# Performance work log

Measured on AMD Instinct MI355X. Metric: run time of the kernel, lower is better.

## Reference

```python
import jax, jax.numpy as jnp
import numpy as np

N0, N1, N2 = 60000, 15000, 3750
K, P = 32, 15
R0 = 0.5  # kernel extent at level 0; doubles per level (first_subsampling_dl*deform_radius scaled to unit-cube data)


def kpconv(q_pts, s_pts, neigh_idx, feats, kpoints, W, extent):
    """Rigid KPConv. q_pts [Nq,3], s_pts [Ns,3], neigh_idx [Nq,K] (shadow=Ns),
    feats [Ns,Cin], kpoints [P,3] unit-scale, W [P,Cin,Cout]."""
    s_pts_p = jnp.concatenate([s_pts, jnp.full((1, 3), 1e6, s_pts.dtype)], 0)
    feats_p = jnp.concatenate([feats, jnp.zeros((1, feats.shape[1]), feats.dtype)], 0)
    neigh_pts = s_pts_p[neigh_idx]                       # [Nq,K,3] gather
    neigh_f = feats_p[neigh_idx]                         # [Nq,K,Cin] gather
    diff = neigh_pts - q_pts[:, None, :]                 # [Nq,K,3]
    dist = jnp.sqrt(jnp.sum((diff[:, :, None, :] - kpoints[None, None] * extent) ** 2, -1))
    infl = jnp.maximum(0.0, 1.0 - dist / extent)         # [Nq,K,P] linear influence
    fk = jnp.einsum('nkp,nkc->npc', infl, neigh_f)       # per-kernel-point aggregation
    out = jnp.einsum('npc,pco->no', fk, W)
    return jax.nn.leaky_relu(out, 0.1)


def detection_scores(neighbor, features):
    # verbatim translation of KPFCNN.detection_scores (eval mode)
    n_total = features.shape[0]
    feats = jnp.concatenate([features, jnp.zeros_like(features[:1])], 0)
    neighbor = jnp.concatenate([neighbor, jnp.full_like(neighbor[:1], n_total)], 0)
    feats = feats / (jnp.max(feats) + 1e-6)
    nf = feats[neighbor]                                 # [N+1,K,C]
    nnum = jnp.maximum(jnp.sum(jnp.sum(nf, -1) != 0, -1, keepdims=True), 1)
    mean_f = jnp.sum(nf, 1) / nnum
    local_max_score = jax.nn.softplus(feats - mean_f)
    depth_max = jnp.max(feats, 1, keepdims=True)
    all_scores = local_max_score * (feats / (1e-6 + depth_max))
    scores = jnp.max(all_scores, 1, keepdims=True)
    detected = jnp.max((feats == jnp.max(nf, 1)).astype(feats.dtype), 1, keepdims=True)
    return (scores * detected)[:-1]


def reference(features, points0, points1, points2, neighbors0, neighbors1, neighbors2,
              pools0, pools1, upsamples0, upsamples1, kpoints, W1, W2, W3, W4, W5, Wu1, Wu2):
    # ---- encoder ----
    f = kpconv(points0, points0, neighbors0, features, kpoints, W1, R0)      # simple         [N0,64]
    skip0 = f
    f = kpconv(points1, points0, pools0, f, kpoints, W2, R0)                 # simple_strided [N1,64]
    f = kpconv(points1, points1, neighbors1, f, kpoints, W3, 2 * R0)         # simple         [N1,128]
    skip1 = f
    f = kpconv(points2, points1, pools1, f, kpoints, W4, 2 * R0)             # simple_strided [N2,128]
    f = kpconv(points2, points2, neighbors2, f, kpoints, W5, 4 * R0)         # simple         [N2,256]
    # ---- decoder: nearest_upsample + skip concat + unary ----
    f = jnp.concatenate([f[upsamples1[:, 0]], skip1], 1)                     # [N1,384] (1.5*256)
    f = jax.nn.leaky_relu(f @ Wu1, 0.1)                                      # unary          [N1,128]
    f = jnp.concatenate([f[upsamples0[:, 0]], skip0], 1)                     # [N0,192]
    f = f @ Wu2                                                              # last_unary     [N0,32]
    scores = detection_scores(neighbors0, f)
    fnorm = f / jnp.maximum(jnp.linalg.norm(f, axis=-1, keepdims=True), 1e-12)
    return fnorm, scores


def setup_inputs() -> dict:
    key = jax.random.key(0)
    ks = jax.random.split(key, 20)
    inp = {
        'features': jax.random.normal(ks[0], (N0, 1), jnp.float32),
        'points0': jax.random.uniform(ks[1], (N0, 3), jnp.float32),
        'points1': jax.random.uniform(ks[2], (N1, 3), jnp.float32),
        'points2': jax.random.uniform(ks[3], (N2, 3), jnp.float32),
        'neighbors0': jax.random.randint(ks[4], (N0, K), 0, N0, jnp.int32),
        'neighbors1': jax.random.randint(ks[5], (N1, K), 0, N1, jnp.int32),
        'neighbors2': jax.random.randint(ks[6], (N2, K), 0, N2, jnp.int32),
        'pools0': jax.random.randint(ks[7], (N1, K), 0, N0, jnp.int32),
        'pools1': jax.random.randint(ks[8], (N2, K), 0, N1, jnp.int32),
        'upsamples0': jax.random.randint(ks[9], (N0, 1), 0, N1, jnp.int32),
        'upsamples1': jax.random.randint(ks[10], (N1, 1), 0, N2, jnp.int32),
        'kpoints': jax.random.normal(ks[11], (P, 3), jnp.float32) * 0.5,
    }
    def w(k, shape, fan_in):
        return jax.random.normal(k, shape, jnp.float32) / np.sqrt(fan_in)
    inp['W1'] = w(ks[12], (P, 1, 64), P * 1)
    inp['W2'] = w(ks[13], (P, 64, 64), P * 64)
    inp['W3'] = w(ks[14], (P, 64, 128), P * 64)
    inp['W4'] = w(ks[15], (P, 128, 128), P * 128)
    inp['W5'] = w(ks[16], (P, 128, 256), P * 128)
    inp['Wu1'] = w(ks[17], (384, 128), 384)
    inp['Wu2'] = w(ks[18], (192, 32), 192)
    return inp
```

## Files before the change

### kernel.cpp

```cpp
#include <hip/hip_runtime.h>
#include <math.h>

static const int cN0 = 60000;
static const int cN1 = 15000;
static const int cN2 = 3750;

typedef __bf16 bf16x8 __attribute__((ext_vector_type(8)));
typedef float f32x4 __attribute__((ext_vector_type(4)));

#define GLOAD_LDS16(gsrc, ldst)                                                        \
  __builtin_amdgcn_global_load_lds((const __attribute__((address_space(1))) void*)(gsrc), \
                                   (__attribute__((address_space(3))) void*)(ldst), 16, 0, 0)

__global__ __launch_bounds__(256) void prep_kernel(
    const float* __restrict__ pts0, const float* __restrict__ feat,
    const float* __restrict__ pts1, const float* __restrict__ pts2,
    const float* __restrict__ W2, const float* __restrict__ W3, const float* __restrict__ W4,
    const float* __restrict__ W5, const float* __restrict__ Wu1, const float* __restrict__ Wu2,
    float4* __restrict__ pk0, float4* __restrict__ pk1, float4* __restrict__ pk2,
    __bf16* __restrict__ T2, __bf16* __restrict__ T3, __bf16* __restrict__ T4,
    __bf16* __restrict__ T5, __bf16* __restrict__ Tu1, __bf16* __restrict__ Tu2) {
  int role = blockIdx.y;
  int tid = blockIdx.x * 256 + threadIdx.x;
  int stride = gridDim.x * 256;
  if (role < 3) {
    const float* p = role == 0 ? pts0 : (role == 1 ? pts1 : pts2);
    float4* o = role == 0 ? pk0 : (role == 1 ? pk1 : pk2);
    int n = role == 0 ? cN0 : (role == 1 ? cN1 : cN2);
    for (int i = tid; i < n; i += stride) {
      float4 v;
      v.x = p[(size_t)i * 3 + 0];
      v.y = p[(size_t)i * 3 + 1];
      v.z = p[(size_t)i * 3 + 2];
      v.w = role == 0 ? feat[i] : 0.f;
      o[i] = v;
    }
  } else {
    const float* src;
    __bf16* dst;
    int Kd, Nd;
    switch (role) {
      case 3: src = W2;  dst = T2;  Kd = 960;  Nd = 64;  break;
      case 4: src = W3;  dst = T3;  Kd = 960;  Nd = 128; break;
      case 5: src = W4;  dst = T4;  Kd = 1920; Nd = 128; break;
      case 6: src = W5;  dst = T5;  Kd = 1920; Nd = 256; break;
      case 7: src = Wu1; dst = Tu1; Kd = 384;  Nd = 128; break;
      default: src = Wu2; dst = Tu2; Kd = 192; Nd = 32;  break;
    }
    int total = Kd * Nd;
    for (int e = tid; e < total; e += stride) {
      int n = e / Kd, k = e % Kd;
      dst[e] = (__bf16)src[(size_t)k * Nd + n];
    }
  }
}

__global__ __launch_bounds__(256) void kpconv_l1(
    const float4* __restrict__ pk, const int* __restrict__ neigh,
    const float* __restrict__ kpts, const float* __restrict__ W1,
    __bf16* __restrict__ f0, float extent) {
  const int t = threadIdx.x;
  const int n0b = blockIdx.x * 16;
  __shared__ float s_nb[32][16][4];
  __shared__ float s_fk[16][16];
  __shared__ float s_W[960];
  for (int i = t; i < 960; i += 256) s_W[i] = W1[i];
  #pragma unroll
  for (int i = 0; i < 2; ++i) {
    int e = t + i * 256;
    int pt = e & 15, k = e >> 4;
    int idx = neigh[(size_t)(n0b + pt) * 32 + k];
    *(float4*)&s_nb[k][pt][0] = pk[idx];
  }
  __syncthreads();
  const int lane = t & 63, wave = t >> 6;
  const int g = lane >> 4, p_raw = lane & 15;
  const int p = p_raw < 15 ? p_raw : 0;
  const int pt = wave * 4 + g;
  const int n = n0b + pt;
  const float inv = 1.f / extent;
  float4 q = pk[n];
  const float kx = q.x + kpts[p * 3 + 0] * extent;
  const float ky = q.y + kpts[p * 3 + 1] * extent;
  const float kz = q.z + kpts[p * 3 + 2] * extent;
  float fk = 0.f;
  #pragma unroll 8
  for (int k = 0; k < 32; ++k) {
    f32x4 rec = *(const f32x4*)&s_nb[k][pt][0];
    float dx = rec[0] - kx, dy = rec[1] - ky, dz = rec[2] - kz;
    float d = sqrtf(dx * dx + dy * dy + dz * dz);
    fk += fmaxf(0.f, 1.f - d * inv) * rec[3];
  }
  if (p_raw < 15) s_fk[pt][p_raw] = fk;
  __syncthreads();
  #pragma unroll
  for (int o = 0; o < 4; ++o) {
    int e = o * 256 + t;
    int opt = e >> 6, c = e & 63;
    float acc = 0.f;
    #pragma unroll
    for (int pp = 0; pp < 15; ++pp) acc += s_fk[opt][pp] * s_W[pp * 64 + c];
    acc = acc > 0.f ? acc : 0.1f * acc;
    f0[(size_t)(n0b + opt) * 64 + c] = (__bf16)acc;
  }
}

template <int CIN, int PTS>
__global__ __launch_bounds__(256) void kpconv_agg_mfma(
    const float4* __restrict__ qp, const float4* __restrict__ sp,
    const int* __restrict__ neigh, const __bf16* __restrict__ F,
    const float* __restrict__ kpts, __bf16* __restrict__ fkb,
    int M, float extent) {
  constexpr int ROWS = PTS * 32;
  constexpr int TPR = 256 / ROWS;
  constexpr int CPT = CIN / (8 * TPR);
  constexpr int NCC = CIN / 16;
  constexpr int PPW = PTS / 4;
  __shared__ __bf16 s_F[PTS][32][CIN];
  __shared__ __bf16 s_infl[PTS][16][40];
  const int t = threadIdx.x;
  const int rowid = t / TPR, half = t % TPR;
  const int pt = rowid >> 5, k = rowid & 31;
  const int n = blockIdx.x * PTS + pt;
  const int n_eff = n < M ? n : M - 1;
  const int idx = neigh[(size_t)n_eff * 32 + k];
  {
    const __bf16* src = F + (size_t)idx * CIN + half * (CIN / TPR);
    __bf16* dst = &s_F[pt][k][half * (CIN / TPR)];
    #pragma unroll
    for (int j = 0; j < CPT; ++j) *(bf16x8*)(dst + j * 8) = *(const bf16x8*)(src + j * 8);
  }
  {
    float4 q = qp[n_eff];
    float4 s = sp[idx];
    float sx = s.x - q.x, sy = s.y - q.y, sz = s.z - q.z;
    float inv = 1.f / extent;
    #pragma unroll
    for (int p = 0; p < 15; ++p) {
      float dx = sx - kpts[p * 3 + 0] * extent;
      float dy = sy - kpts[p * 3 + 1] * extent;
      float dz = sz - kpts[p * 3 + 2] * extent;
      float d = sqrtf(dx * dx + dy * dy + dz * dz);
      s_infl[pt][p][k] = (__bf16)fmaxf(0.f, 1.f - d * inv);
    }
  }
  __syncthreads();
  const int lane = t & 63, wave = t >> 6;
  const int g = lane >> 4, c16 = lane & 15;
  #pragma unroll
  for (int qq = 0; qq < PPW; ++qq) {
    const int lpt = wave * PPW + qq;
    const int nn = blockIdx.x * PTS + lpt;
    bf16x8 a = *(const bf16x8*)&s_infl[lpt][c16][g * 8];
    if (nn < M) {
      const size_t base = (size_t)nn * (15 * CIN);
      #pragma unroll
      for (int cc = 0; cc < NCC; ++cc) {
        bf16x8 b;
        #pragma unroll
        for (int j = 0; j < 8; ++j) b[j] = s_F[lpt][g * 8 + j][cc * 16 + c16];
        f32x4 acc = __builtin_amdgcn_mfma_f32_16x16x32_bf16(a, b, (f32x4){0.f, 0.f, 0.f, 0.f}, 0, 0, 0);
        #pragma unroll
        for (int r = 0; r < 4; ++r) {
          int p = g * 4 + r;
          if (p < 15) fkb[base + (size_t)p * CIN + cc * 16 + c16] = (__bf16)acc[r];
        }
      }
    }
  }
}

template <bool LEAKY, bool GATHER, bool OUTF32, bool MAXOUT>
__global__ __launch_bounds__(256, 2) void gemm_mfma(
    const __bf16* __restrict__ A1, const __bf16* __restrict__ A2,
    const int* __restrict__ gidx, const int K1,
    const __bf16* __restrict__ BT, void* __restrict__ Cout,
    const int M, const int N, const int KK, unsigned* __restrict__ gmax) {
  __shared__ __bf16 sA[2][4096];
  __shared__ __bf16 sB[2][4096];
  __shared__ float s_max[4];
  const int t = threadIdx.x;
  const int lane = t & 63, wave = t >> 6;
  const int wr = wave >> 1, wc = wave & 1;
  const int m0 = blockIdx.y * 64, n0 = blockIdx.x * 64;
  const int K2 = KK - K1;

  const __bf16* a1row[2];
  const __bf16* a2row[2];
  const __bf16* brow_[2];
  int csrc[2], wbase[2];
  #pragma unroll
  for (int r = 0; r < 2; ++r) {
    int slot = r * 256 + wave * 64 + lane;
    int row = slot >> 3;
    csrc[r] = ((slot & 7) ^ (row & 7)) * 8;
    wbase[r] = (r * 256 + wave * 64) * 8;
    int gm = m0 + row; if (gm > M - 1) gm = M - 1;
    if (GATHER) {
      a1row[r] = A1 + (size_t)gidx[gm] * K1;
      a2row[r] = A2 + (size_t)gm * (size_t)K2;
    } else {
      a1row[r] = A1 + (size_t)gm * (size_t)KK;
    }
    int gn = n0 + row; if (gn > N - 1) gn = N - 1;
    brow_[r] = BT + (size_t)gn * (size_t)KK;
  }

  int offA[2][2], offB[2][2];
  #pragma unroll
  for (int i = 0; i < 2; ++i)
    #pragma unroll
    for (int s = 0; s < 2; ++s) {
      int ra = wr * 32 + i * 16 + (lane & 15);
      int rb = wc * 32 + i * 16 + (lane & 15);
      int ch = s * 4 + (lane >> 4);
      offA[i][s] = ra * 64 + (ch ^ (ra & 7)) * 8;
      offB[i][s] = rb * 64 + (ch ^ (rb & 7)) * 8;
    }

  f32x4 acc[2][2];
  #pragma unroll
  for (int i = 0; i < 2; ++i)
    #pragma unroll
    for (int j = 0; j < 2; ++j) acc[i][j] = (f32x4){0.f, 0.f, 0.f, 0.f};

  auto stage = [&](int buf, int k0) {
    #pragma unroll
    for (int r = 0; r < 2; ++r) {
      int kg = k0 + csrc[r];
      const __bf16* asrc;
      if (GATHER) asrc = (kg < K1) ? (a1row[r] + kg) : (a2row[r] + (kg - K1));
      else        asrc = a1row[r] + kg;
      GLOAD_LDS16(asrc, &sA[buf][wbase[r]]);
      GLOAD_LDS16(brow_[r] + kg, &sB[buf][wbase[r]]);
    }
  };

  stage(0, 0);
  __syncthreads();
  const int nk = KK >> 6;
  int cur = 0;
  for (int kt = 0; kt < nk; ++kt) {
    if (kt + 1 < nk) stage(cur ^ 1, (kt + 1) << 6);
    #pragma unroll
    for (int s = 0; s < 2; ++s) {
      bf16x8 a0 = *(const bf16x8*)&sA[cur][offA[0][s]];
      bf16x8 a1 = *(const bf16x8*)&sA[cur][offA[1][s]];
      bf16x8 b0 = *(const bf16x8*)&sB[cur][offB[0][s]];
      bf16x8 b1 = *(const bf16x8*)&sB[cur][offB[1][s]];
      acc[0][0] = __builtin_amdgcn_mfma_f32_16x16x32_bf16(a0, b0, acc[0][0], 0, 0, 0);
      acc[0][1] = __builtin_amdgcn_mfma_f32_16x16x32_bf16(a0, b1, acc[0][1], 0, 0, 0);
      acc[1][0] = __builtin_amdgcn_mfma_f32_16x16x32_bf16(a1, b0, acc[1][0], 0, 0, 0);
      acc[1][1] = __builtin_amdgcn_mfma_f32_16x16x32_bf16(a1, b1, acc[1][1], 0, 0, 0);
    }
    __syncthreads();
    cur ^= 1;
  }

  float lmax = 0.f;
  #pragma unroll
  for (int i = 0; i < 2; ++i)
    #pragma unroll
    for (int j = 0; j < 2; ++j)
      #pragma unroll
      for (int g = 0; g < 4; ++g) {
        int row = m0 + wr * 32 + i * 16 + (lane >> 4) * 4 + g;
        int col = n0 + wc * 32 + j * 16 + (lane & 15);
        if (row < M && col < N) {
          float v = acc[i][j][g];
          if (LEAKY) v = v > 0.f ? v : 0.1f * v;
          if (MAXOUT) lmax = fmaxf(lmax, v);
          if (OUTF32) ((float*)Cout)[(size_t)row * N + col] = v;
          else        ((__bf16*)Cout)[(size_t)row * N + col] = (__bf16)v;
        }
      }
  if (MAXOUT) {
    #pragma unroll
    for (int s = 32; s >= 1; s >>= 1) lmax = fmaxf(lmax, __shfl_xor(lmax, s, 64));
    if (lane == 0) s_max[wave] = lmax;
    __syncthreads();
    if (t == 0) {
      float mm = fmaxf(fmaxf(s_max[0], s_max[1]), fmaxf(s_max[2], s_max[3]));
      atomicMax(gmax, __float_as_uint(mm));
    }
  }
}

__global__ __launch_bounds__(256) void detect_kernel(
    const float* __restrict__ f6, const int* __restrict__ neigh,
    const float* __restrict__ gm_ptr, float* __restrict__ out_fnorm,
    float* __restrict__ out_scores, int N) {
  int n = blockIdx.x * 8 + (threadIdx.x >> 5);
  int c = threadIdx.x & 31;
  if (n >= N) return;
  float denom = gm_ptr[0] + 1e-6f;
  float fown = f6[(size_t)n * 32 + c];
  int idx_l = neigh[(size_t)n * 32 + c];
  float colsum = 0.f, colmax = -1e30f;
  for (int k = 0; k < 32; ++k) {
    int idx = __shfl(idx_l, k, 32);
    float v = f6[(size_t)idx * 32 + c];
    colsum += v;
    colmax = fmaxf(colmax, v);
  }
  float fs = fown / denom;
  float mean = (colsum / denom) * (1.f / 32.f);
  float x = fs - mean;
  float lms = fmaxf(x, 0.f) + log1pf(expf(-fabsf(x)));
  float dm = fs;
  #pragma unroll
  for (int s = 16; s >= 1; s >>= 1) dm = fmaxf(dm, __shfl_xor(dm, s, 32));
  float as = lms * fs / (1e-6f + dm);
  float sc = as;
  #pragma unroll
  for (int s = 16; s >= 1; s >>= 1) sc = fmaxf(sc, __shfl_xor(sc, s, 32));
  float det = (fown == colmax) ? 1.f : 0.f;
  #pragma unroll
  for (int s = 16; s >= 1; s >>= 1) det = fmaxf(det, __shfl_xor(det, s, 32));
  float nn2 = fown * fown;
  #pragma unroll
  for (int s = 16; s >= 1; s >>= 1) nn2 += __shfl_xor(nn2, s, 32);
  float inv_nrm = 1.f / fmaxf(sqrtf(nn2), 1e-12f);
  out_fnorm[(size_t)n * 32 + c] = fown * inv_nrm;
  if (c == 0) out_scores[n] = sc * det;
}

extern "C" void kernel_launch(void* const* d_in, const int* in_sizes, int n_in,
                              void* d_out, int out_size, void* d_ws, size_t ws_size,
                              hipStream_t stream) {
  const float* features  = (const float*)d_in[0];
  const float* points0   = (const float*)d_in[1];
  const float* points1   = (const float*)d_in[2];
  const float* points2   = (const float*)d_in[3];
  const int* neighbors0  = (const int*)d_in[4];
  const int* neighbors1  = (const int*)d_in[5];
  const int* neighbors2  = (const int*)d_in[6];
  const int* pools0      = (const int*)d_in[7];
  const int* pools1      = (const int*)d_in[8];
  const int* upsamples0  = (const int*)d_in[9];
  const int* upsamples1  = (const int*)d_in[10];
  const float* kpoints   = (const float*)d_in[11];
  const float* W1  = (const float*)d_in[12];
  const float* W2  = (const float*)d_in[13];
  const float* W3  = (const float*)d_in[14];
  const float* W4  = (const float*)d_in[15];
  const float* W5  = (const float*)d_in[16];
  const float* Wu1 = (const float*)d_in[17];
  const float* Wu2 = (const float*)d_in[18];

  const float R0 = 0.5f;

  char* wp = (char*)d_ws;
  auto alloc = [&](size_t bytes) {
    char* r = wp;
    wp += (bytes + 255) & ~(size_t)255;
    return r;
  };
  __bf16* f0b  = (__bf16*)alloc((size_t)cN0 * 64 * 2);
  __bf16* f1b  = (__bf16*)alloc((size_t)cN1 * 64 * 2);
  __bf16* f2b  = (__bf16*)alloc((size_t)cN1 * 128 * 2);
  __bf16* f3b  = (__bf16*)alloc((size_t)cN2 * 128 * 2);
  __bf16* f4b  = (__bf16*)alloc((size_t)cN2 * 256 * 2);
  __bf16* f5b  = (__bf16*)alloc((size_t)cN1 * 128 * 2);
  float*  f6   = (float*)alloc((size_t)cN0 * 32 * 4);
  __bf16* WT2  = (__bf16*)alloc(960 * 64 * 2);
  __bf16* WT3  = (__bf16*)alloc(960 * 128 * 2);
  __bf16* WT4  = (__bf16*)alloc(1920 * 128 * 2);
  __bf16* WT5  = (__bf16*)alloc(1920 * 256 * 2);
  __bf16* WTu1 = (__bf16*)alloc(384 * 128 * 2);
  __bf16* WTu2 = (__bf16*)alloc(192 * 32 * 2);
  unsigned* gm = (unsigned*)alloc(256);
  float4* pk0  = (float4*)alloc((size_t)cN0 * 16);
  float4* pk1  = (float4*)alloc((size_t)cN1 * 16);
  float4* pk2  = (float4*)alloc((size_t)cN2 * 16);
  __bf16* fkb  = (__bf16*)alloc((size_t)cN1 * 960 * 2);

  prep_kernel<<<dim3(240, 9), 256, 0, stream>>>(
      points0, features, points1, points2, W2, W3, W4, W5, Wu1, Wu2,
      pk0, pk1, pk2, WT2, WT3, WT4, WT5, WTu1, WTu2);
  kpconv_l1<<<cN0 / 16, 256, 0, stream>>>(pk0, neighbors0, kpoints, W1, f0b, R0);

  kpconv_agg_mfma<64, 8><<<cN1 / 8, 256, 0, stream>>>(pk1, pk0, pools0, f0b, kpoints, fkb, cN1, R0);
  gemm_mfma<true, false, false, false><<<dim3(1, 235), 256, 0, stream>>>(
      fkb, nullptr, nullptr, 0, WT2, f1b, cN1, 64, 960, nullptr);
  kpconv_agg_mfma<64, 8><<<cN1 / 8, 256, 0, stream>>>(pk1, pk1, neighbors1, f1b, kpoints, fkb, cN1, 2.f * R0);
  gemm_mfma<true, false, false, false><<<dim3(2, 235), 256, 0, stream>>>(
      fkb, nullptr, nullptr, 0, WT3, f2b, cN1, 128, 960, nullptr);
  kpconv_agg_mfma<128, 4><<<(cN2 + 3) / 4, 256, 0, stream>>>(pk2, pk1, pools1, f2b, kpoints, fkb, cN2, 2.f * R0);
  gemm_mfma<true, false, false, false><<<dim3(2, 59), 256, 0, stream>>>(
      fkb, nullptr, nullptr, 0, WT4, f3b, cN2, 128, 1920, nullptr);
  kpconv_agg_mfma<128, 4><<<(cN2 + 3) / 4, 256, 0, stream>>>(pk2, pk2, neighbors2, f3b, kpoints, fkb, cN2, 4.f * R0);
  gemm_mfma<true, false, false, false><<<dim3(4, 59), 256, 0, stream>>>(
      fkb, nullptr, nullptr, 0, WT5, f4b, cN2, 256, 1920, nullptr);
  gemm_mfma<true, true, false, false><<<dim3(2, 235), 256, 0, stream>>>(
      f4b, f2b, upsamples1, 256, WTu1, f5b, cN1, 128, 384, nullptr);
  hipMemsetAsync(gm, 0, 4, stream);
  gemm_mfma<false, true, true, true><<<dim3(1, 938), 256, 0, stream>>>(
      f5b, f0b, upsamples0, 128, WTu2, f6, cN0, 32, 192, gm);

  float* out_fnorm = (float*)d_out;
  float* out_scores = out_fnorm + (size_t)cN0 * 32;
  detect_kernel<<<(cN0 + 7) / 8, 256, 0, stream>>>(f6, neighbors0, (const float*)gm,
                                                   out_fnorm, out_scores, cN0);
}
```

Before: 224.6 us.

## Fuse KPConv aggregation and weight GEMM into one kernel per layer

```diff
diff --git a/kernel.cpp b/kernel.cpp
--- a/kernel.cpp
+++ b/kernel.cpp
@@ -105,69 +105,214 @@
   }
 }
 
-template <int CIN, int PTS>
-__global__ __launch_bounds__(256) void kpconv_agg_mfma(
+template <int CIN, int COUT, int BM, bool BDBUF>
+__global__ __launch_bounds__(512) void kpconv_fused(
     const float4* __restrict__ qp, const float4* __restrict__ sp,
     const int* __restrict__ neigh, const __bf16* __restrict__ F,
-    const float* __restrict__ kpts, __bf16* __restrict__ fkb,
-    int M, float extent) {
-  constexpr int ROWS = PTS * 32;
-  constexpr int TPR = 256 / ROWS;
-  constexpr int CPT = CIN / (8 * TPR);
-  constexpr int NCC = CIN / 16;
-  constexpr int PPW = PTS / 4;
-  __shared__ __bf16 s_F[PTS][32][CIN];
-  __shared__ __bf16 s_infl[PTS][16][40];
+    const float* __restrict__ kpts, const __bf16* __restrict__ BT,
+    __bf16* __restrict__ out, int M, float extent) {
+  constexpr int KK = 15 * CIN;
+  constexpr int KT = KK / 64;
+  constexpr int CPRow = CIN / 8;
+  constexpr int RPB = 8192 / CIN;
+  constexpr int GS = RPB / 2;
+  constexpr int BP = RPB / 32;
+  constexpr int NB = BM * 32 / RPB;
+  constexpr int WPP = 8 / BP;
+  constexpr int FBUF = 8192;
+  constexpr int RG = BM / 16;
+  constexpr int CG = 8 / RG;
+  constexpr int NJ = COUT / (16 * CG);
+  constexpr int SMEM_FK = BM * KK * 2;
+  constexpr int SMEM = SMEM_FK + BP * 1280 + BM * 16 + 2 * FBUF * 2;
+
+  __shared__ __align__(16) char smem[SMEM];
+  __bf16* s_fk   = (__bf16*)smem;
+  __bf16* s_infl = (__bf16*)(smem + SMEM_FK);
+  float4* s_q    = (float4*)(smem + SMEM_FK + BP * 1280);
+  __bf16* s_F    = (__bf16*)(smem + SMEM_FK + BP * 1280 + BM * 16);
+  __bf16* s_B    = s_F;
+
   const int t = threadIdx.x;
-  const int rowid = t / TPR, half = t % TPR;
-  const int pt = rowid >> 5, k = rowid & 31;
-  const int n = blockIdx.x * PTS + pt;
-  const int n_eff = n < M ? n : M - 1;
-  const int idx = neigh[(size_t)n_eff * 32 + k];
-  {
-    const __bf16* src = F + (size_t)idx * CIN + half * (CIN / TPR);
-    __bf16* dst = &s_F[pt][k][half * (CIN / TPR)];
-    #pragma unroll
-    for (int j = 0; j < CPT; ++j) *(bf16x8*)(dst + j * 8) = *(const bf16x8*)(src + j * 8);
-  }
-  {
-    float4 q = qp[n_eff];
-    float4 s = sp[idx];
-    float sx = s.x - q.x, sy = s.y - q.y, sz = s.z - q.z;
-    float inv = 1.f / extent;
-    #pragma unroll
-    for (int p = 0; p < 15; ++p) {
-      float dx = sx - kpts[p * 3 + 0] * extent;
-      float dy = sy - kpts[p * 3 + 1] * extent;
-      float dz = sz - kpts[p * 3 + 2] * extent;
+  const int w = t >> 6, l = t & 63;
+  const int c16 = l & 15, g4 = l >> 4;
+  const int m0 = blockIdx.x * BM;
+  const int* nb_base = neigh + (size_t)m0 * 32;
+  int rlim = (M - m0) * 32 - 1;
+  if (rlim > BM * 32 - 1) rlim = BM * 32 - 1;
+
+  const int gb = t / CPRow;
+  const int ch = t % CPRow;
+  int idxg[NB][2];
+  #pragma unroll
+  for (int b = 0; b < NB; ++b)
+    #pragma unroll
+    for (int j = 0; j < 2; ++j) {
+      int r = b * RPB + gb + j * GS;
+      idxg[b][j] = nb_base[r < rlim ? r : rlim];
+    }
+  const int ii  = t & 1;
+  const int pq4 = ((t >> 1) & 3) * 4;
+  const int row_i = gb + ii * GS;
+  const int pt_i = row_i >> 5, kk_i = row_i & 31;
+  const float inv = 1.f / extent;
+  float kpx[4], kpy[4], kpz[4];
+  #pragma unroll
+  for (int pi = 0; pi < 4; ++pi) {
+    int p = pq4 + pi; if (p > 14) p = 14;
+    kpx[pi] = kpts[p * 3 + 0] * extent;
+    kpy[pi] = kpts[p * 3 + 1] * extent;
+    kpz[pi] = kpts[p * 3 + 2] * extent;
+  }
+  if (t < BM) { int n = m0 + t; s_q[t] = qp[n < M ? n : M - 1]; }
+
+  auto stageF = [&](int buf, const int (&ig)[2]) {
+    #pragma unroll
+    for (int j = 0; j < 2; ++j) {
+      int k = (gb + j * GS) & 31;
+      const __bf16* src = F + (size_t)ig[j] * CIN + (ch ^ ((k >> 3) & 3)) * 8;
+      GLOAD_LDS16(src, s_F + buf * FBUF + (j * 512 + t) * 8);
+    }
+  };
+  auto inflC = [&](const float4& spv, int b, float (&v)[4]) {
+    float4 q = s_q[b * BP + pt_i];
+    float sx = spv.x - q.x, sy = spv.y - q.y, sz = spv.z - q.z;
+    #pragma unroll
+    for (int pi = 0; pi < 4; ++pi) {
+      float dx = sx - kpx[pi], dy = sy - kpy[pi], dz = sz - kpz[pi];
       float d = sqrtf(dx * dx + dy * dy + dz * dz);
-      s_infl[pt][p][k] = (__bf16)fmaxf(0.f, 1.f - d * inv);
-    }
-  }
-  __syncthreads();
-  const int lane = t & 63, wave = t >> 6;
-  const int g = lane >> 4, c16 = lane & 15;
-  #pragma unroll
-  for (int qq = 0; qq < PPW; ++qq) {
-    const int lpt = wave * PPW + qq;
-    const int nn = blockIdx.x * PTS + lpt;
-    bf16x8 a = *(const bf16x8*)&s_infl[lpt][c16][g * 8];
-    if (nn < M) {
-      const size_t base = (size_t)nn * (15 * CIN);
+      v[pi] = fmaxf(0.f, 1.f - d * inv);
+    }
+  };
+  auto inflStore = [&](const float (&v)[4]) {
+    #pragma unroll
+    for (int pi = 0; pi < 4; ++pi) {
+      int p = pq4 + pi;
+      if (p < 15) s_infl[pt_i * 640 + p * 40 + kk_i] = (__bf16)v[pi];
+    }
+  };
+  auto mfmaBatch = [&](int b, int buf) {
+    const int pt_loc = w / WPP;
+    const int cc0 = (w % WPP) * 2;
+    const __bf16* Fb = s_F + buf * FBUF + pt_loc * (32 * CIN);
+    bf16x8 a = *(const bf16x8*)&s_infl[pt_loc * 640 + c16 * 40 + g4 * 8];
+    const int row = b * BP + pt_loc;
+    #pragma unroll
+    for (int ci = 0; ci < 2; ++ci) {
+      const int cc = cc0 + ci;
+      const int Lc = cc * 2 + (c16 >> 3);
+      const int pc = Lc ^ g4;
+      bf16x8 bv;
       #pragma unroll
-      for (int cc = 0; cc < NCC; ++cc) {
-        bf16x8 b;
-        #pragma unroll
-        for (int j = 0; j < 8; ++j) b[j] = s_F[lpt][g * 8 + j][cc * 16 + c16];
-        f32x4 acc = __builtin_amdgcn_mfma_f32_16x16x32_bf16(a, b, (f32x4){0.f, 0.f, 0.f, 0.f}, 0, 0, 0);
-        #pragma unroll
-        for (int r = 0; r < 4; ++r) {
-          int p = g * 4 + r;
-          if (p < 15) fkb[base + (size_t)p * CIN + cc * 16 + c16] = (__bf16)acc[r];
+      for (int j = 0; j < 8; ++j)
+        bv[j] = Fb[(g4 * 8 + j) * CIN + pc * 8 + (c16 & 7)];
+      f32x4 acc = __builtin_amdgcn_mfma_f32_16x16x32_bf16(a, bv, (f32x4){0.f, 0.f, 0.f, 0.f}, 0, 0, 0);
+      #pragma unroll
+      for (int r = 0; r < 4; ++r) {
+        int p = g4 * 4 + r;
+        if (p < 15) {
+          int Lf = p * CPRow + Lc;
+          int phys = (Lf & ~7) | ((Lf & 7) ^ (row & 7));
+          s_fk[(size_t)row * KK + phys * 8 + (c16 & 7)] = (__bf16)acc[r];
         }
       }
     }
-  }
+  };
+
+  asm volatile("s_waitcnt lgkmcnt(0)" ::: "memory");
+  __builtin_amdgcn_s_barrier();
+  __builtin_amdgcn_sched_barrier(0);
+
+  float4 spc, spn;
+  {
+    float4 sp0 = sp[idxg[0][ii]];
+    stageF(0, idxg[0]);
+    spc = sp[idxg[NB > 1 ? 1 : 0][ii]];
+    float v0[4];
+    inflC(sp0, 0, v0);
+    inflStore(v0);
+  }
+  __builtin_amdgcn_sched_barrier(0);
+  #pragma unroll
+  for (int b = 0; b < NB; ++b) {
+    if (b + 1 < NB) stageF((b + 1) & 1, idxg[b + 1]);
+    if (b + 2 < NB) spn = sp[idxg[b + 2][ii]];
+    float vn[4];
+    if (b + 1 < NB) inflC(spc, b + 1, vn);
+    if (b + 1 < NB) { asm volatile("s_waitcnt vmcnt(3)" ::: "memory"); }
+    else            { asm volatile("s_waitcnt vmcnt(0)" ::: "memory"); }
+    asm volatile("s_waitcnt lgkmcnt(0)" ::: "memory");
+    __builtin_amdgcn_s_barrier();
+    __builtin_amdgcn_sched_barrier(0);
+    mfmaBatch(b, b & 1);
+    asm volatile("s_waitcnt lgkmcnt(0)" ::: "memory");
+    __builtin_amdgcn_s_barrier();
+    __builtin_amdgcn_sched_barrier(0);
+    if (b + 1 < NB) { inflStore(vn); spc = spn; }
+  }
+  __syncthreads();
+
+  const int wr = w / CG, wc = w % CG;
+  f32x4 acc[NJ];
+  #pragma unroll
+  for (int j = 0; j < NJ; ++j) acc[j] = (f32x4){0.f, 0.f, 0.f, 0.f};
+  auto stageB = [&](int buf, int kt) {
+    #pragma unroll
+    for (int rnd = 0; rnd < COUT / 64; ++rnd) {
+      int slot = rnd * 512 + t;
+      int row = slot >> 3, bch = slot & 7;
+      GLOAD_LDS16(BT + (size_t)row * KK + kt * 64 + (bch ^ (row & 7)) * 8,
+                  s_B + buf * (COUT * 64) + slot * 8);
+    }
+  };
+  const __bf16* fkrow = s_fk + (size_t)(wr * 16 + c16) * KK;
+  auto computeTile = [&](int kt, int buf) {
+    bf16x8 af[2];
+    #pragma unroll
+    for (int s = 0; s < 2; ++s)
+      af[s] = *(const bf16x8*)&fkrow[((kt * 8 + (s * 4 + g4)) & ~7 | (((s * 4 + g4) & 7) ^ (c16 & 7))) * 8 + (kt * 8 & ~7) * 0];
+    #pragma unroll
+    for (int s = 0; s < 2; ++s)
+      af[s] = *(const bf16x8*)&fkrow[(kt * 8 + ((s * 4 + g4) ^ (c16 & 7))) * 8];
+    const __bf16* Bb = s_B + buf * (COUT * 64);
+    #pragma unroll
+    for (int j = 0; j < NJ; ++j) {
+      int n = wc * (16 * NJ) + j * 16 + c16;
+      #pragma unroll
+      for (int s = 0; s < 2; ++s) {
+        bf16x8 bf = *(const bf16x8*)&Bb[n * 64 + ((s * 4 + g4) ^ (n & 7)) * 8];
+        acc[j] = __builtin_amdgcn_mfma_f32_16x16x32_bf16(af[s], bf, acc[j], 0, 0, 0);
+      }
+    }
+  };
+  if (BDBUF) {
+    stageB(0, 0);
+    __syncthreads();
+    for (int kt = 0; kt < KT; ++kt) {
+      if (kt + 1 < KT) stageB((kt + 1) & 1, kt + 1);
+      computeTile(kt, kt & 1);
+      __syncthreads();
+    }
+  } else {
+    for (int kt = 0; kt < KT; ++kt) {
+      stageB(0, kt);
+      __syncthreads();
+      computeTile(kt, 0);
+      __syncthreads();
+    }
+  }
+  #pragma unroll
+  for (int j = 0; j < NJ; ++j)
+    #pragma unroll
+    for (int r = 0; r < 4; ++r) {
+      int row = m0 + wr * 16 + g4 * 4 + r;
+      int col = wc * (16 * NJ) + j * 16 + c16;
+      if (row < M) {
+        float v = acc[j][r];
+        v = v > 0.f ? v : 0.1f * v;
+        out[(size_t)row * COUT + col] = (__bf16)v;
+      }
+    }
 }
 
 template <bool LEAKY, bool GATHER, bool OUTF32, bool MAXOUT>
@@ -213,9 +358,9 @@
     for (int s = 0; s < 2; ++s) {
       int ra = wr * 32 + i * 16 + (lane & 15);
       int rb = wc * 32 + i * 16 + (lane & 15);
-      int ch = s * 4 + (lane >> 4);
-      offA[i][s] = ra * 64 + (ch ^ (ra & 7)) * 8;
-      offB[i][s] = rb * 64 + (ch ^ (rb & 7)) * 8;
+      int chn = s * 4 + (lane >> 4);
+      offA[i][s] = ra * 64 + (chn ^ (ra & 7)) * 8;
+      offB[i][s] = rb * 64 + (chn ^ (rb & 7)) * 8;
     }
 
   f32x4 acc[2][2];
@@ -373,25 +518,21 @@
   float4* pk0  = (float4*)alloc((size_t)cN0 * 16);
   float4* pk1  = (float4*)alloc((size_t)cN1 * 16);
   float4* pk2  = (float4*)alloc((size_t)cN2 * 16);
-  __bf16* fkb  = (__bf16*)alloc((size_t)cN1 * 960 * 2);
 
   prep_kernel<<<dim3(240, 9), 256, 0, stream>>>(
       points0, features, points1, points2, W2, W3, W4, W5, Wu1, Wu2,
       pk0, pk1, pk2, WT2, WT3, WT4, WT5, WTu1, WTu2);
   kpconv_l1<<<cN0 / 16, 256, 0, stream>>>(pk0, neighbors0, kpoints, W1, f0b, R0);
 
-  kpconv_agg_mfma<64, 8><<<cN1 / 8, 256, 0, stream>>>(pk1, pk0, pools0, f0b, kpoints, fkb, cN1, R0);
-  gemm_mfma<true, false, false, false><<<dim3(1, 235), 256, 0, stream>>>(
-      fkb, nullptr, nullptr, 0, WT2, f1b, cN1, 64, 960, nullptr);
-  kpconv_agg_mfma<64, 8><<<cN1 / 8, 256, 0, stream>>>(pk1, pk1, neighbors1, f1b, kpoints, fkb, cN1, 2.f * R0);
-  gemm_mfma<true, false, false, false><<<dim3(2, 235), 256, 0, stream>>>(
-      fkb, nullptr, nullptr, 0, WT3, f2b, cN1, 128, 960, nullptr);
-  kpconv_agg_mfma<128, 4><<<(cN2 + 3) / 4, 256, 0, stream>>>(pk2, pk1, pools1, f2b, kpoints, fkb, cN2, 2.f * R0);
-  gemm_mfma<true, false, false, false><<<dim3(2, 59), 256, 0, stream>>>(
-      fkb, nullptr, nullptr, 0, WT4, f3b, cN2, 128, 1920, nullptr);
-  kpconv_agg_mfma<128, 4><<<(cN2 + 3) / 4, 256, 0, stream>>>(pk2, pk2, neighbors2, f3b, kpoints, fkb, cN2, 4.f * R0);
-  gemm_mfma<true, false, false, false><<<dim3(4, 59), 256, 0, stream>>>(
-      fkb, nullptr, nullptr, 0, WT5, f4b, cN2, 256, 1920, nullptr);
+  kpconv_fused<64, 64, 64, true><<<(cN1 + 63) / 64, 512, 0, stream>>>(
+      pk1, pk0, pools0, f0b, kpoints, WT2, f1b, cN1, R0);
+  kpconv_fused<64, 128, 64, true><<<(cN1 + 63) / 64, 512, 0, stream>>>(
+      pk1, pk1, neighbors1, f1b, kpoints, WT3, f2b, cN1, 2.f * R0);
+  kpconv_fused<128, 128, 16, true><<<(cN2 + 15) / 16, 512, 0, stream>>>(
+      pk2, pk1, pools1, f2b, kpoints, WT4, f3b, cN2, 2.f * R0);
+  kpconv_fused<128, 256, 16, false><<<(cN2 + 15) / 16, 512, 0, stream>>>(
+      pk2, pk2, neighbors2, f3b, kpoints, WT5, f4b, cN2, 4.f * R0);
+
   gemm_mfma<true, true, false, false><<<dim3(2, 235), 256, 0, stream>>>(
       f4b, f2b, upsamples1, 256, WTu1, f5b, cN1, 128, 384, nullptr);
   hipMemsetAsync(gm, 0, 4, stream);
```

Result: faster. 219.1 us (-2.4%).
